# Performance work log

Hardware: AMD Instinct MI355X
Metric: run time of the kernel (lower is better)

## Reference

```python
import jax, jax.numpy as jnp
import numpy as np

BN = 100000
E = 1600000
C1 = 64
C2 = 64


def setup_inputs() -> dict:
    key = jax.random.key(0)
    k1, k2, k3, k4 = jax.random.split(key, 4)
    x = jax.random.normal(k1, (BN, C1), dtype=jnp.float32)
    e_ = jax.random.randint(k2, (2, E), 0, BN, dtype=jnp.int64)
    # nn.Linear(C1, C2): y = x @ W^T + b; store W pre-transposed as (C1, C2)
    W = jax.random.normal(k3, (C1, C2), dtype=jnp.float32) * (1.0 / np.sqrt(C1))
    b = jax.random.normal(k4, (C2,), dtype=jnp.float32) * 0.01
    return {"x": x, "e_": e_, "W": W, "b": b}


def reference(x, e_, W, b):
    bn = x.shape[0]
    row, col = e_[0], e_[1]
    # deg = bincount(row); deg^{-1/2} with inf -> 0
    deg = jax.ops.segment_sum(jnp.ones(row.shape, dtype=x.dtype), row, num_segments=bn)
    deg_inv_sqrt = jnp.where(deg > 0, jnp.power(jnp.maximum(deg, 1.0), -0.5), 0.0)
    norm = deg_inv_sqrt[row] * deg_inv_sqrt[col]          # (E,)
    h = x @ W + b                                         # (BN, C2)
    messages = norm[:, None] * h[row]                     # (E, C2) gather + scale
    y = jax.ops.segment_sum(messages, col, num_segments=bn)  # scatter-add over dst
    return y
```

## Files before the change

### kernel.cpp

```cpp
#include <hip/hip_runtime.h>
#include <hip/hip_bf16.h>

#define C 64
#define CPB 1024
#define NBUCK 98
#define EPB 4096
#define PAD 16
#define CAP 20480
#define NW 4

typedef __attribute__((ext_vector_type(8))) short bf16x8;
typedef __attribute__((ext_vector_type(4))) float f32x4;

__device__ __forceinline__ unsigned short f2bf(float f) {
    __hip_bfloat16 h = __float2bfloat16(f);
    return *(unsigned short*)&h;
}

__global__ void init_kernel(int* __restrict__ bcC, int* __restrict__ bcR) {
    int t = threadIdx.x;
    if (t < NBUCK) { bcC[t * PAD] = t * CAP; bcR[t * PAD] = t * CAP; }
}

__global__ __launch_bounds__(256) void partA_kernel(const int* __restrict__ row,
                                                    const int* __restrict__ col,
                                                    int* __restrict__ bcurC,
                                                    int* __restrict__ bcurR,
                                                    int* __restrict__ stageC,
                                                    unsigned short* __restrict__ stageR,
                                                    int ne) {
    __shared__ int cC[NW][NBUCK], cR[NW][NBUCK];
    const int tid = threadIdx.x;
    const int w = tid >> 6;
    for (int i = tid; i < NW * NBUCK; i += 256) { (&cC[0][0])[i] = 0; (&cR[0][0])[i] = 0; }
    __syncthreads();
    int s = blockIdx.x * EPB, e = min(s + EPB, ne);
    for (int i = s + tid; i < e; i += 256) {
        atomicAdd(&cC[w][col[i] >> 10], 1);
        atomicAdd(&cR[w][row[i] >> 10], 1);
    }
    __syncthreads();
    if (tid < NBUCK) {
        int tot = 0;
#pragma unroll
        for (int k = 0; k < NW; ++k) tot += cC[k][tid];
        int g = atomicAdd(&bcurC[tid * PAD], tot);
#pragma unroll
        for (int k = 0; k < NW; ++k) { int t2 = cC[k][tid]; cC[k][tid] = g; g += t2; }
        tot = 0;
#pragma unroll
        for (int k = 0; k < NW; ++k) tot += cR[k][tid];
        g = atomicAdd(&bcurR[tid * PAD], tot);
#pragma unroll
        for (int k = 0; k < NW; ++k) { int t2 = cR[k][tid]; cR[k][tid] = g; g += t2; }
    }
    __syncthreads();
    for (int i = s + tid; i < e; i += 256) {
        int r = row[i], c = col[i];
        int bk = c >> 10;
        int pos = atomicAdd(&cC[w][bk], 1);
        if (pos < (bk + 1) * CAP) stageC[pos] = ((c & (CPB - 1)) << 17) | r;
        int rb = r >> 10;
        int posR = atomicAdd(&cR[w][rb], 1);
        if (posR < (rb + 1) * CAP) stageR[posR] = (unsigned short)(r & (CPB - 1));
    }
}

__global__ void scanb_kernel(const int* __restrict__ bcC, int* __restrict__ bboff) {
    if (threadIdx.x == 0) {
        int acc = 0;
        for (int b = 0; b < NBUCK; ++b) {
            bboff[b] = acc;
            acc += bcC[b * PAD] - b * CAP;
        }
        bboff[NBUCK] = acc;
    }
}

__global__ __launch_bounds__(1024) void degB_kernel(const int* __restrict__ bcR,
                                                    const unsigned short* __restrict__ stageR,
                                                    float* __restrict__ dis, int bn) {
    __shared__ int hist[CPB];
    const int b = blockIdx.x, tid = threadIdx.x;
    hist[tid] = 0;
    __syncthreads();
    const int sb = b * CAP;
    const int cnt = bcR[b * PAD] - sb;
    for (int j = tid; j < cnt; j += 1024) atomicAdd(&hist[stageR[sb + j]], 1);
    __syncthreads();
    int r = b * CPB + tid;
    if (r < bn) {
        int d = hist[tid];
        dis[r] = d > 0 ? rsqrtf((float)d) : 0.0f;
    }
}

__global__ __launch_bounds__(1024) void partB_kernel(const int* __restrict__ bboff,
                                                     const int* __restrict__ stageC,
                                                     int* __restrict__ offs,
                                                     int* __restrict__ srcs,
                                                     int bn, int ne) {
    __shared__ int hist[CPB];
    __shared__ int wsum[16];
    const int b = blockIdx.x, tid = threadIdx.x;
    const int lane = tid & 63, wid = tid >> 6;
    hist[tid] = 0;
    __syncthreads();
    const int s = bboff[b];
    const int cnt = bboff[b + 1] - s;
    const int sb = b * CAP;
    for (int j = tid; j < cnt; j += 1024) atomicAdd(&hist[stageC[sb + j] >> 17], 1);
    __syncthreads();
    int v = hist[tid];
    int x = v;
#pragma unroll
    for (int off = 1; off < 64; off <<= 1) {
        int t = __shfl_up(x, off, 64);
        if (lane >= off) x += t;
    }
    if (lane == 63) wsum[wid] = x;
    __syncthreads();
    if (wid == 0) {
        int ws2 = (lane < 16) ? wsum[lane] : 0;
        int y = ws2;
#pragma unroll
        for (int off = 1; off < 16; off <<= 1) {
            int t = __shfl_up(y, off, 64);
            if (lane >= off) y += t;
        }
        if (lane < 16) wsum[lane] = y - ws2;
    }
    __syncthreads();
    int excl = (x - v) + wsum[wid];
    int c = b * CPB + tid;
    if (c < bn) offs[c] = s + excl;
    __syncthreads();
    hist[tid] = s + excl;
    __syncthreads();
    for (int j = tid; j < cnt; j += 1024) {
        int val = stageC[sb + j];
        int pos = atomicAdd(&hist[val >> 17], 1);
        srcs[pos] = val & 0x1FFFF;
    }
    if (b == NBUCK - 1 && tid == 0) offs[bn] = ne;
}

__global__ __launch_bounds__(256) void linear_mfma_kernel(const float* __restrict__ x,
                                                          const float* __restrict__ W,
                                                          const float* __restrict__ b,
                                                          const float* __restrict__ dis,
                                                          __hip_bfloat16* __restrict__ hb,
                                                          int bn) {
    __shared__ unsigned short xb[64][72];
    __shared__ unsigned short Wt[64][72];
    __shared__ float bs[64];
    __shared__ float dss[64];
    const int t = threadIdx.x;
    const int R0 = blockIdx.x * 64;

    {
        int row = t >> 2, q = t & 3;
        int grow = R0 + row;
        float4 vv[4];
        if (grow < bn) {
            const float4* xp = (const float4*)(x + (size_t)grow * C + q * 16);
#pragma unroll
            for (int i = 0; i < 4; ++i) vv[i] = xp[i];
        } else {
#pragma unroll
            for (int i = 0; i < 4; ++i) vv[i] = make_float4(0.f, 0.f, 0.f, 0.f);
        }
#pragma unroll
        for (int i = 0; i < 4; ++i) {
            unsigned short* d = &xb[row][q * 16 + i * 4];
            d[0] = f2bf(vv[i].x); d[1] = f2bf(vv[i].y);
            d[2] = f2bf(vv[i].z); d[3] = f2bf(vv[i].w);
        }
    }
    {
        int k = t >> 2, q = t & 3;
        const float* wp = W + (size_t)k * C + q * 16;
#pragma unroll
        for (int j = 0; j < 16; ++j) Wt[q * 16 + j][k] = f2bf(wp[j]);
    }
    if (t < 64) bs[t] = b[t];
    else if (t < 128) { int i = t - 64; int g = R0 + i; dss[i] = (g < bn) ? dis[g] : 0.f; }
    __syncthreads();

    const int wv = t >> 6;
    const int l = t & 63;
    const int lm = l & 15;
    const int g = l >> 4;

    const bf16x8 a0 = *(const bf16x8*)&xb[wv * 16 + lm][g * 8];
    const bf16x8 a1 = *(const bf16x8*)&xb[wv * 16 + lm][32 + g * 8];

#pragma unroll
    for (int n = 0; n < 4; ++n) {
        const bf16x8 b0 = *(const bf16x8*)&Wt[n * 16 + lm][g * 8];
        const bf16x8 b1 = *(const bf16x8*)&Wt[n * 16 + lm][32 + g * 8];
        float bias = bs[n * 16 + lm];
        f32x4 acc = {bias, bias, bias, bias};
        acc = __builtin_amdgcn_mfma_f32_16x16x32_bf16(a0, b0, acc, 0, 0, 0);
        acc = __builtin_amdgcn_mfma_f32_16x16x32_bf16(a1, b1, acc, 0, 0, 0);
#pragma unroll
        for (int reg = 0; reg < 4; ++reg) {
            int lrow = wv * 16 + g * 4 + reg;
            int grow = R0 + lrow;
            if (grow < bn)
                hb[(size_t)grow * C + n * 16 + lm] = __float2bfloat16(dss[lrow] * acc[reg]);
        }
    }
}

__device__ __forceinline__ float bf_lo(unsigned int p) { return __uint_as_float(p << 16); }
__device__ __forceinline__ float bf_hi(unsigned int p) { return __uint_as_float(p & 0xFFFF0000u); }

__global__ void gather_kernel(const int* __restrict__ offs, const int* __restrict__ srcs,
                              const uint2* __restrict__ hb64,
                              const float* __restrict__ dis,
                              float* __restrict__ y, int bn) {
    int r = blockIdx.x * (blockDim.x >> 6) + (threadIdx.x >> 6);
    if (r >= bn) return;
    const int lane = threadIdx.x & 63;
    const int q = lane >> 4;
    const int cq = lane & 15;
    const int s0 = offs[r], e0 = offs[r + 1];
    float4 acc = {0.f, 0.f, 0.f, 0.f};
    for (int base = s0; base < e0; base += 64) {
        int j = base + lane;
        int srcv = (j < e0) ? srcs[j] : 0;
        int cnt = min(64, e0 - base);
        int t = 0;
        for (; t + 16 <= cnt; t += 16) {
            int a0 = __shfl(srcv, t + q, 64);
            int a1 = __shfl(srcv, t + 4 + q, 64);
            int a2 = __shfl(srcv, t + 8 + q, 64);
            int a3 = __shfl(srcv, t + 12 + q, 64);
            uint2 p0 = hb64[(size_t)a0 * 16 + cq];
            uint2 p1 = hb64[(size_t)a1 * 16 + cq];
            uint2 p2 = hb64[(size_t)a2 * 16 + cq];
            uint2 p3 = hb64[(size_t)a3 * 16 + cq];
            acc.x += bf_lo(p0.x); acc.y += bf_hi(p0.x); acc.z += bf_lo(p0.y); acc.w += bf_hi(p0.y);
            acc.x += bf_lo(p1.x); acc.y += bf_hi(p1.x); acc.z += bf_lo(p1.y); acc.w += bf_hi(p1.y);
            acc.x += bf_lo(p2.x); acc.y += bf_hi(p2.x); acc.z += bf_lo(p2.y); acc.w += bf_hi(p2.y);
            acc.x += bf_lo(p3.x); acc.y += bf_hi(p3.x); acc.z += bf_lo(p3.y); acc.w += bf_hi(p3.y);
        }
        for (; t + 4 <= cnt; t += 4) {
            int a = __shfl(srcv, t + q, 64);
            uint2 p = hb64[(size_t)a * 16 + cq];
            acc.x += bf_lo(p.x); acc.y += bf_hi(p.x); acc.z += bf_lo(p.y); acc.w += bf_hi(p.y);
        }
        if (t < cnt) {
            int idx = t + q;
            int a = __shfl(srcv, idx & 63, 64);
            if (idx < cnt) {
                uint2 p = hb64[(size_t)a * 16 + cq];
                acc.x += bf_lo(p.x); acc.y += bf_hi(p.x); acc.z += bf_lo(p.y); acc.w += bf_hi(p.y);
            }
        }
    }
    acc.x += __shfl_xor(acc.x, 16, 64); acc.y += __shfl_xor(acc.y, 16, 64);
    acc.z += __shfl_xor(acc.z, 16, 64); acc.w += __shfl_xor(acc.w, 16, 64);
    acc.x += __shfl_xor(acc.x, 32, 64); acc.y += __shfl_xor(acc.y, 32, 64);
    acc.z += __shfl_xor(acc.z, 32, 64); acc.w += __shfl_xor(acc.w, 32, 64);
    if (q == 0) {
        float d = dis[r];
        float4 out = {acc.x * d, acc.y * d, acc.z * d, acc.w * d};
        *reinterpret_cast<float4*>(y + (size_t)r * C + 4 * cq) = out;
    }
}

extern "C" void kernel_launch(void* const* d_in, const int* in_sizes, int n_in,
                              void* d_out, int out_size, void* d_ws, size_t ws_size,
                              hipStream_t stream) {
    const float* x = (const float*)d_in[0];
    const int*   e = (const int*)d_in[1];
    const float* W = (const float*)d_in[2];
    const float* b = (const float*)d_in[3];
    float* y = (float*)d_out;

    const int bn = in_sizes[0] / C;
    const int ne = in_sizes[1] / 2;

    const int* rowi = e;
    const int* coli = e + ne;

    char* ws = (char*)d_ws;
    float* dis   = (float*)ws;  ws += (size_t)bn * 4;
    int*   offs  = (int*)ws;    ws += ((size_t)bn + 4) * 4;
    int*   bboff = (int*)ws;    ws += 512;
    int*   bcC   = (int*)ws;    ws += (size_t)NBUCK * PAD * 4;
    int*   bcR   = (int*)ws;    ws += (size_t)NBUCK * PAD * 4;
    int*   srcs  = (int*)ws;    ws += (size_t)ne * 4;
    __hip_bfloat16* hb = (__hip_bfloat16*)ws;
    int*            stageC = (int*)hb;
    unsigned short* stageR = (unsigned short*)((char*)hb + (size_t)NBUCK * CAP * 4);

    const int nchunks = (ne + EPB - 1) / EPB;
    init_kernel<<<1, 128, 0, stream>>>(bcC, bcR);
    partA_kernel<<<nchunks, 256, 0, stream>>>(rowi, coli, bcC, bcR, stageC, stageR, ne);
    degB_kernel<<<NBUCK, 1024, 0, stream>>>(bcR, stageR, dis, bn);
    scanb_kernel<<<1, 64, 0, stream>>>(bcC, bboff);
    partB_kernel<<<NBUCK, 1024, 0, stream>>>(bboff, stageC, offs, srcs, bn, ne);
    linear_mfma_kernel<<<(bn + 63) / 64, 256, 0, stream>>>(x, W, b, dis, hb, bn);
    gather_kernel<<<(bn + 3) / 4, 256, 0, stream>>>(offs, srcs, (const uint2*)hb, dis, y, bn);
}
```

Baseline: 148.5 us.

## Use finer 256-node buckets across partition, degree and CSR build kernels

Shrinks the bucket width from 1024 to 256 nodes, so there are 391 buckets instead of 98 and the degree and partB kernels launch four times as many smaller blocks. This is meant to fill more compute units during the bucket passes. PartA now preloads 16 edges per thread into registers, drops the per-wave counter copies, and stores row-degree staging as bytes. The serial single-thread bucket scan becomes a parallel wave scan. In exchange, more blocks contend on the same global bucket counters, and shared-memory atomics become more contended without the per-wave copies.

After: 135.1 us. -9.0%, faster.

```diff
diff --git a/kernel.cpp b/kernel.cpp
--- a/kernel.cpp
+++ b/kernel.cpp
@@ -2,12 +2,11 @@
 #include <hip/hip_bf16.h>
 
 #define C 64
-#define CPB 1024
-#define NBUCK 98
+#define CPB 256
+#define NBUCK 391
 #define EPB 4096
 #define PAD 16
-#define CAP 20480
-#define NW 4
+#define CAP 5120
 
 typedef __attribute__((ext_vector_type(8))) short bf16x8;
 typedef __attribute__((ext_vector_type(4))) float f32x4;
@@ -17,7 +16,7 @@
     return *(unsigned short*)&h;
 }
 
-__global__ void init_kernel(int* __restrict__ bcC, int* __restrict__ bcR) {
+__global__ __launch_bounds__(512) void init_kernel(int* __restrict__ bcC, int* __restrict__ bcR) {
     int t = threadIdx.x;
     if (t < NBUCK) { bcC[t * PAD] = t * CAP; bcR[t * PAD] = t * CAP; }
 }
@@ -27,66 +26,85 @@
                                                     int* __restrict__ bcurC,
                                                     int* __restrict__ bcurR,
                                                     int* __restrict__ stageC,
-                                                    unsigned short* __restrict__ stageR,
+                                                    unsigned char* __restrict__ stageR,
                                                     int ne) {
-    __shared__ int cC[NW][NBUCK], cR[NW][NBUCK];
+    __shared__ int cC[NBUCK], cR[NBUCK];
     const int tid = threadIdx.x;
-    const int w = tid >> 6;
-    for (int i = tid; i < NW * NBUCK; i += 256) { (&cC[0][0])[i] = 0; (&cR[0][0])[i] = 0; }
-    __syncthreads();
-    int s = blockIdx.x * EPB, e = min(s + EPB, ne);
-    for (int i = s + tid; i < e; i += 256) {
-        atomicAdd(&cC[w][col[i] >> 10], 1);
-        atomicAdd(&cR[w][row[i] >> 10], 1);
-    }
-    __syncthreads();
-    if (tid < NBUCK) {
-        int tot = 0;
-#pragma unroll
-        for (int k = 0; k < NW; ++k) tot += cC[k][tid];
-        int g = atomicAdd(&bcurC[tid * PAD], tot);
-#pragma unroll
-        for (int k = 0; k < NW; ++k) { int t2 = cC[k][tid]; cC[k][tid] = g; g += t2; }
-        tot = 0;
-#pragma unroll
-        for (int k = 0; k < NW; ++k) tot += cR[k][tid];
-        g = atomicAdd(&bcurR[tid * PAD], tot);
-#pragma unroll
-        for (int k = 0; k < NW; ++k) { int t2 = cR[k][tid]; cR[k][tid] = g; g += t2; }
-    }
-    __syncthreads();
-    for (int i = s + tid; i < e; i += 256) {
-        int r = row[i], c = col[i];
-        int bk = c >> 10;
-        int pos = atomicAdd(&cC[w][bk], 1);
-        if (pos < (bk + 1) * CAP) stageC[pos] = ((c & (CPB - 1)) << 17) | r;
-        int rb = r >> 10;
-        int posR = atomicAdd(&cR[w][rb], 1);
-        if (posR < (rb + 1) * CAP) stageR[posR] = (unsigned short)(r & (CPB - 1));
-    }
-}
-
-__global__ void scanb_kernel(const int* __restrict__ bcC, int* __restrict__ bboff) {
-    if (threadIdx.x == 0) {
-        int acc = 0;
-        for (int b = 0; b < NBUCK; ++b) {
-            bboff[b] = acc;
-            acc += bcC[b * PAD] - b * CAP;
-        }
-        bboff[NBUCK] = acc;
-    }
-}
-
-__global__ __launch_bounds__(1024) void degB_kernel(const int* __restrict__ bcR,
-                                                    const unsigned short* __restrict__ stageR,
-                                                    float* __restrict__ dis, int bn) {
+    for (int i = tid; i < NBUCK; i += 256) { cC[i] = 0; cR[i] = 0; }
+    __syncthreads();
+    const int s = blockIdx.x * EPB, e = min(s + EPB, ne);
+    int rr[16], cc[16];
+#pragma unroll
+    for (int u = 0; u < 16; ++u) {
+        int i = s + tid + u * 256;
+        if (i < e) { rr[u] = row[i]; cc[u] = col[i]; }
+        else { rr[u] = -1; cc[u] = -1; }
+    }
+#pragma unroll
+    for (int u = 0; u < 16; ++u) {
+        if (cc[u] >= 0) {
+            atomicAdd(&cC[cc[u] >> 8], 1);
+            atomicAdd(&cR[rr[u] >> 8], 1);
+        }
+    }
+    __syncthreads();
+    for (int t = tid; t < NBUCK; t += 256) {
+        int g = atomicAdd(&bcurC[t * PAD], cC[t]); cC[t] = g;
+        g = atomicAdd(&bcurR[t * PAD], cR[t]); cR[t] = g;
+    }
+    __syncthreads();
+#pragma unroll
+    for (int u = 0; u < 16; ++u) {
+        if (cc[u] >= 0) {
+            int bk = cc[u] >> 8;
+            int pos = atomicAdd(&cC[bk], 1);
+            if (pos < (bk + 1) * CAP) stageC[pos] = ((cc[u] & 255) << 17) | rr[u];
+            int rb = rr[u] >> 8;
+            int posR = atomicAdd(&cR[rb], 1);
+            if (posR < (rb + 1) * CAP) stageR[posR] = (unsigned char)(rr[u] & 255);
+        }
+    }
+}
+
+__global__ __launch_bounds__(512) void scanb_kernel(const int* __restrict__ bcC,
+                                                    int* __restrict__ bboff) {
+    __shared__ int wsum[8];
+    const int tid = threadIdx.x, lane = tid & 63, wid = tid >> 6;
+    int v = (tid < NBUCK) ? min(bcC[tid * PAD] - tid * CAP, CAP) : 0;
+    int x = v;
+#pragma unroll
+    for (int off = 1; off < 64; off <<= 1) {
+        int t = __shfl_up(x, off, 64);
+        if (lane >= off) x += t;
+    }
+    if (lane == 63) wsum[wid] = x;
+    __syncthreads();
+    if (wid == 0) {
+        int ws2 = (lane < 8) ? wsum[lane] : 0;
+        int y = ws2;
+#pragma unroll
+        for (int off = 1; off < 8; off <<= 1) {
+            int t = __shfl_up(y, off, 64);
+            if (lane >= off) y += t;
+        }
+        if (lane < 8) wsum[lane] = y - ws2;
+    }
+    __syncthreads();
+    int excl = (x - v) + wsum[wid];
+    if (tid < NBUCK) bboff[tid] = excl;
+    if (tid == NBUCK - 1) bboff[NBUCK] = excl + v;
+}
+
+__global__ __launch_bounds__(256) void degB_kernel(const int* __restrict__ bcR,
+                                                   const unsigned char* __restrict__ stageR,
+                                                   float* __restrict__ dis, int bn) {
     __shared__ int hist[CPB];
     const int b = blockIdx.x, tid = threadIdx.x;
     hist[tid] = 0;
     __syncthreads();
     const int sb = b * CAP;
-    const int cnt = bcR[b * PAD] - sb;
-    for (int j = tid; j < cnt; j += 1024) atomicAdd(&hist[stageR[sb + j]], 1);
+    const int cnt = min(bcR[b * PAD] - sb, CAP);
+    for (int j = tid; j < cnt; j += 256) atomicAdd(&hist[stageR[sb + j]], 1);
     __syncthreads();
     int r = b * CPB + tid;
     if (r < bn) {
@@ -95,23 +113,23 @@
     }
 }
 
-__global__ __launch_bounds__(1024) void partB_kernel(const int* __restrict__ bboff,
-                                                     const int* __restrict__ stageC,
-                                                     int* __restrict__ offs,
-                                                     int* __restrict__ srcs,
-                                                     int bn, int ne) {
+__global__ __launch_bounds__(512) void partB_kernel(const int* __restrict__ bboff,
+                                                    const int* __restrict__ stageC,
+                                                    int* __restrict__ offs,
+                                                    int* __restrict__ srcs,
+                                                    int bn, int ne) {
     __shared__ int hist[CPB];
-    __shared__ int wsum[16];
+    __shared__ int wsum[8];
     const int b = blockIdx.x, tid = threadIdx.x;
     const int lane = tid & 63, wid = tid >> 6;
-    hist[tid] = 0;
+    if (tid < CPB) hist[tid] = 0;
     __syncthreads();
     const int s = bboff[b];
     const int cnt = bboff[b + 1] - s;
     const int sb = b * CAP;
-    for (int j = tid; j < cnt; j += 1024) atomicAdd(&hist[stageC[sb + j] >> 17], 1);
-    __syncthreads();
-    int v = hist[tid];
+    for (int j = tid; j < cnt; j += 512) atomicAdd(&hist[stageC[sb + j] >> 17], 1);
+    __syncthreads();
+    int v = (tid < CPB) ? hist[tid] : 0;
     int x = v;
 #pragma unroll
     for (int off = 1; off < 64; off <<= 1) {
@@ -121,23 +139,23 @@
     if (lane == 63) wsum[wid] = x;
     __syncthreads();
     if (wid == 0) {
-        int ws2 = (lane < 16) ? wsum[lane] : 0;
+        int ws2 = (lane < 8) ? wsum[lane] : 0;
         int y = ws2;
 #pragma unroll
-        for (int off = 1; off < 16; off <<= 1) {
+        for (int off = 1; off < 8; off <<= 1) {
             int t = __shfl_up(y, off, 64);
             if (lane >= off) y += t;
         }
-        if (lane < 16) wsum[lane] = y - ws2;
+        if (lane < 8) wsum[lane] = y - ws2;
     }
     __syncthreads();
     int excl = (x - v) + wsum[wid];
     int c = b * CPB + tid;
-    if (c < bn) offs[c] = s + excl;
-    __syncthreads();
-    hist[tid] = s + excl;
-    __syncthreads();
-    for (int j = tid; j < cnt; j += 1024) {
+    if (tid < CPB && c < bn) offs[c] = s + excl;
+    __syncthreads();
+    if (tid < CPB) hist[tid] = s + excl;
+    __syncthreads();
+    for (int j = tid; j < cnt; j += 512) {
         int val = stageC[sb + j];
         int pos = atomicAdd(&hist[val >> 17], 1);
         srcs[pos] = val & 0x1FFFF;
@@ -289,20 +307,20 @@
     char* ws = (char*)d_ws;
     float* dis   = (float*)ws;  ws += (size_t)bn * 4;
     int*   offs  = (int*)ws;    ws += ((size_t)bn + 4) * 4;
-    int*   bboff = (int*)ws;    ws += 512;
+    int*   bboff = (int*)ws;    ws += ((size_t)NBUCK + 4) * 4;
     int*   bcC   = (int*)ws;    ws += (size_t)NBUCK * PAD * 4;
     int*   bcR   = (int*)ws;    ws += (size_t)NBUCK * PAD * 4;
     int*   srcs  = (int*)ws;    ws += (size_t)ne * 4;
     __hip_bfloat16* hb = (__hip_bfloat16*)ws;
-    int*            stageC = (int*)hb;
-    unsigned short* stageR = (unsigned short*)((char*)hb + (size_t)NBUCK * CAP * 4);
+    int*           stageC = (int*)hb;
+    unsigned char* stageR = (unsigned char*)((char*)hb + (size_t)NBUCK * CAP * 4);
 
     const int nchunks = (ne + EPB - 1) / EPB;
-    init_kernel<<<1, 128, 0, stream>>>(bcC, bcR);
+    init_kernel<<<1, 512, 0, stream>>>(bcC, bcR);
     partA_kernel<<<nchunks, 256, 0, stream>>>(rowi, coli, bcC, bcR, stageC, stageR, ne);
-    degB_kernel<<<NBUCK, 1024, 0, stream>>>(bcR, stageR, dis, bn);
-    scanb_kernel<<<1, 64, 0, stream>>>(bcC, bboff);
-    partB_kernel<<<NBUCK, 1024, 0, stream>>>(bboff, stageC, offs, srcs, bn, ne);
+    degB_kernel<<<NBUCK, 256, 0, stream>>>(bcR, stageR, dis, bn);
+    scanb_kernel<<<1, 512, 0, stream>>>(bcC, bboff);
+    partB_kernel<<<NBUCK, 512, 0, stream>>>(bboff, stageC, offs, srcs, bn, ne);
     linear_mfma_kernel<<<(bn + 63) / 64, 256, 0, stream>>>(x, W, b, dis, hb, bn);
     gather_kernel<<<(bn + 3) / 4, 256, 0, stream>>>(offs, srcs, (const uint2*)hb, dis, y, bn);
 }
```

## Use finer buckets and fuse degree, scan and CSR build into one kernel

Applied to the files above, without the earlier changes.

Shrinks the bucket size from 1024 to 128 nodes, giving 782 buckets and 8-bit local row indices in the degree stage. The degree computation, bucket-offset scan and CSR placement are merged into one kernel in which each block computes its own base offset by reducing the counts of earlier buckets. The init and scan kernels are replaced by a memset, partA uses a fixed 512-block grid of 512 threads, and the staging buffers get their own workspace region instead of aliasing hb. The aim is fewer launches and more parallel blocks in the CSR build, at the cost of more global atomics on bucket counters and a redundant prefix sum over earlier buckets in every block.

Result: no change. 150.9 us (+1.6%).

```diff
diff --git a/kernel.cpp b/kernel.cpp
--- a/kernel.cpp
+++ b/kernel.cpp
@@ -2,12 +2,10 @@
 #include <hip/hip_bf16.h>
 
 #define C 64
-#define CPB 1024
-#define NBUCK 98
-#define EPB 4096
+#define CPB 128
+#define NBUCK 782
 #define PAD 16
-#define CAP 20480
-#define NW 4
+#define CAP 2560
 
 typedef __attribute__((ext_vector_type(8))) short bf16x8;
 typedef __attribute__((ext_vector_type(4))) float f32x4;
@@ -17,132 +15,113 @@
     return *(unsigned short*)&h;
 }
 
-__global__ void init_kernel(int* __restrict__ bcC, int* __restrict__ bcR) {
-    int t = threadIdx.x;
-    if (t < NBUCK) { bcC[t * PAD] = t * CAP; bcR[t * PAD] = t * CAP; }
-}
-
-__global__ __launch_bounds__(256) void partA_kernel(const int* __restrict__ row,
+__global__ __launch_bounds__(512) void partA_kernel(const int* __restrict__ row,
                                                     const int* __restrict__ col,
                                                     int* __restrict__ bcurC,
                                                     int* __restrict__ bcurR,
                                                     int* __restrict__ stageC,
-                                                    unsigned short* __restrict__ stageR,
+                                                    unsigned char* __restrict__ stageR,
                                                     int ne) {
-    __shared__ int cC[NW][NBUCK], cR[NW][NBUCK];
+    __shared__ int cC[NBUCK], cR[NBUCK];
     const int tid = threadIdx.x;
-    const int w = tid >> 6;
-    for (int i = tid; i < NW * NBUCK; i += 256) { (&cC[0][0])[i] = 0; (&cR[0][0])[i] = 0; }
-    __syncthreads();
-    int s = blockIdx.x * EPB, e = min(s + EPB, ne);
-    for (int i = s + tid; i < e; i += 256) {
-        atomicAdd(&cC[w][col[i] >> 10], 1);
-        atomicAdd(&cR[w][row[i] >> 10], 1);
-    }
-    __syncthreads();
-    if (tid < NBUCK) {
-        int tot = 0;
-#pragma unroll
-        for (int k = 0; k < NW; ++k) tot += cC[k][tid];
-        int g = atomicAdd(&bcurC[tid * PAD], tot);
-#pragma unroll
-        for (int k = 0; k < NW; ++k) { int t2 = cC[k][tid]; cC[k][tid] = g; g += t2; }
-        tot = 0;
-#pragma unroll
-        for (int k = 0; k < NW; ++k) tot += cR[k][tid];
-        g = atomicAdd(&bcurR[tid * PAD], tot);
-#pragma unroll
-        for (int k = 0; k < NW; ++k) { int t2 = cR[k][tid]; cR[k][tid] = g; g += t2; }
-    }
-    __syncthreads();
-    for (int i = s + tid; i < e; i += 256) {
+    for (int i = tid; i < NBUCK; i += 512) { cC[i] = 0; cR[i] = 0; }
+    __syncthreads();
+    const int per = (ne + gridDim.x - 1) / gridDim.x;
+    const int s = blockIdx.x * per, e = min(s + per, ne);
+    for (int i = s + tid; i < e; i += 512) {
+        atomicAdd(&cC[col[i] >> 7], 1);
+        atomicAdd(&cR[row[i] >> 7], 1);
+    }
+    __syncthreads();
+    for (int t = tid; t < NBUCK; t += 512) {
+        int g = atomicAdd(&bcurC[t * PAD], cC[t]); cC[t] = t * CAP + g;
+        g = atomicAdd(&bcurR[t * PAD], cR[t]);     cR[t] = t * CAP + g;
+    }
+    __syncthreads();
+    for (int i = s + tid; i < e; i += 512) {
         int r = row[i], c = col[i];
-        int bk = c >> 10;
-        int pos = atomicAdd(&cC[w][bk], 1);
-        if (pos < (bk + 1) * CAP) stageC[pos] = ((c & (CPB - 1)) << 17) | r;
-        int rb = r >> 10;
-        int posR = atomicAdd(&cR[w][rb], 1);
-        if (posR < (rb + 1) * CAP) stageR[posR] = (unsigned short)(r & (CPB - 1));
-    }
-}
-
-__global__ void scanb_kernel(const int* __restrict__ bcC, int* __restrict__ bboff) {
-    if (threadIdx.x == 0) {
-        int acc = 0;
-        for (int b = 0; b < NBUCK; ++b) {
-            bboff[b] = acc;
-            acc += bcC[b * PAD] - b * CAP;
-        }
-        bboff[NBUCK] = acc;
-    }
-}
-
-__global__ __launch_bounds__(1024) void degB_kernel(const int* __restrict__ bcR,
-                                                    const unsigned short* __restrict__ stageR,
-                                                    float* __restrict__ dis, int bn) {
-    __shared__ int hist[CPB];
-    const int b = blockIdx.x, tid = threadIdx.x;
-    hist[tid] = 0;
-    __syncthreads();
-    const int sb = b * CAP;
-    const int cnt = bcR[b * PAD] - sb;
-    for (int j = tid; j < cnt; j += 1024) atomicAdd(&hist[stageR[sb + j]], 1);
-    __syncthreads();
-    int r = b * CPB + tid;
-    if (r < bn) {
-        int d = hist[tid];
-        dis[r] = d > 0 ? rsqrtf((float)d) : 0.0f;
-    }
-}
-
-__global__ __launch_bounds__(1024) void partB_kernel(const int* __restrict__ bboff,
+        int bk = c >> 7;
+        int pos = atomicAdd(&cC[bk], 1);
+        if (pos < (bk + 1) * CAP) stageC[pos] = ((c & 127) << 17) | r;
+        int rb = r >> 7;
+        int posR = atomicAdd(&cR[rb], 1);
+        if (posR < (rb + 1) * CAP) stageR[posR] = (unsigned char)(r & 127);
+    }
+}
+
+__global__ __launch_bounds__(512) void fusedB_kernel(const int* __restrict__ bcC,
+                                                     const int* __restrict__ bcR,
                                                      const int* __restrict__ stageC,
+                                                     const unsigned char* __restrict__ stageR,
+                                                     float* __restrict__ dis,
                                                      int* __restrict__ offs,
                                                      int* __restrict__ srcs,
                                                      int bn, int ne) {
     __shared__ int hist[CPB];
-    __shared__ int wsum[16];
+    __shared__ int wsum[8];
+    __shared__ int sbase_s;
     const int b = blockIdx.x, tid = threadIdx.x;
     const int lane = tid & 63, wid = tid >> 6;
-    hist[tid] = 0;
-    __syncthreads();
-    const int s = bboff[b];
-    const int cnt = bboff[b + 1] - s;
-    const int sb = b * CAP;
-    for (int j = tid; j < cnt; j += 1024) atomicAdd(&hist[stageC[sb + j] >> 17], 1);
-    __syncthreads();
-    int v = hist[tid];
-    int x = v;
-#pragma unroll
-    for (int off = 1; off < 64; off <<= 1) {
-        int t = __shfl_up(x, off, 64);
-        if (lane >= off) x += t;
-    }
-    if (lane == 63) wsum[wid] = x;
-    __syncthreads();
-    if (wid == 0) {
-        int ws2 = (lane < 16) ? wsum[lane] : 0;
-        int y = ws2;
-#pragma unroll
-        for (int off = 1; off < 16; off <<= 1) {
-            int t = __shfl_up(y, off, 64);
-            if (lane >= off) y += t;
-        }
-        if (lane < 16) wsum[lane] = y - ws2;
-    }
-    __syncthreads();
-    int excl = (x - v) + wsum[wid];
-    int c = b * CPB + tid;
-    if (c < bn) offs[c] = s + excl;
-    __syncthreads();
-    hist[tid] = s + excl;
-    __syncthreads();
-    for (int j = tid; j < cnt; j += 1024) {
-        int val = stageC[sb + j];
+
+    if (tid < CPB) hist[tid] = 0;
+    __syncthreads();
+    const int sbR = b * CAP;
+    const int cntR = min(bcR[b * PAD], CAP);
+    for (int j = tid; j < cntR; j += 512) atomicAdd(&hist[stageR[sbR + j]], 1);
+    __syncthreads();
+    {
+        int r = b * CPB + tid;
+        if (tid < CPB && r < bn) {
+            int d = hist[tid];
+            dis[r] = d > 0 ? rsqrtf((float)d) : 0.0f;
+        }
+    }
+    int part = 0;
+    for (int t = tid; t < b; t += 512) part += min(bcC[t * PAD], CAP);
+#pragma unroll
+    for (int off = 32; off >= 1; off >>= 1) part += __shfl_xor(part, off, 64);
+    if (lane == 0) wsum[wid] = part;
+    __syncthreads();
+    if (tid == 0) {
+        int s = 0;
+#pragma unroll
+        for (int k = 0; k < 8; ++k) s += wsum[k];
+        sbase_s = s;
+    }
+    __syncthreads();
+    const int sbase = sbase_s;
+    __syncthreads();
+    if (tid < CPB) hist[tid] = 0;
+    __syncthreads();
+    const int sbC = b * CAP;
+    const int cntC = min(bcC[b * PAD], CAP);
+    for (int j = tid; j < cntC; j += 512) atomicAdd(&hist[stageC[sbC + j] >> 17], 1);
+    __syncthreads();
+    int v = 0, x = 0;
+    if (tid < CPB) {
+        v = hist[tid];
+        x = v;
+#pragma unroll
+        for (int off = 1; off < 64; off <<= 1) {
+            int t = __shfl_up(x, off, 64);
+            if (lane >= off) x += t;
+        }
+        if (lane == 63) wsum[wid] = x;
+    }
+    __syncthreads();
+    if (tid < CPB) {
+        int excl = (x - v) + (wid == 1 ? wsum[0] : 0);
+        int c = b * CPB + tid;
+        if (c < bn) offs[c] = sbase + excl;
+        hist[tid] = sbase + excl;
+    }
+    __syncthreads();
+    for (int j = tid; j < cntC; j += 512) {
+        int val = stageC[sbC + j];
         int pos = atomicAdd(&hist[val >> 17], 1);
         srcs[pos] = val & 0x1FFFF;
     }
-    if (b == NBUCK - 1 && tid == 0) offs[bn] = ne;
+    if (b == NBUCK - 1 && tid == 0) offs[bn] = sbase + cntC;
 }
 
 __global__ __launch_bounds__(256) void linear_mfma_kernel(const float* __restrict__ x,
@@ -289,20 +268,17 @@
     char* ws = (char*)d_ws;
     float* dis   = (float*)ws;  ws += (size_t)bn * 4;
     int*   offs  = (int*)ws;    ws += ((size_t)bn + 4) * 4;
-    int*   bboff = (int*)ws;    ws += 512;
     int*   bcC   = (int*)ws;    ws += (size_t)NBUCK * PAD * 4;
     int*   bcR   = (int*)ws;    ws += (size_t)NBUCK * PAD * 4;
     int*   srcs  = (int*)ws;    ws += (size_t)ne * 4;
+    int*           stageC = (int*)ws;           ws += (size_t)NBUCK * CAP * 4;
+    unsigned char* stageR = (unsigned char*)ws; ws += (size_t)NBUCK * CAP;
     __hip_bfloat16* hb = (__hip_bfloat16*)ws;
-    int*            stageC = (int*)hb;
-    unsigned short* stageR = (unsigned short*)((char*)hb + (size_t)NBUCK * CAP * 4);
-
-    const int nchunks = (ne + EPB - 1) / EPB;
-    init_kernel<<<1, 128, 0, stream>>>(bcC, bcR);
-    partA_kernel<<<nchunks, 256, 0, stream>>>(rowi, coli, bcC, bcR, stageC, stageR, ne);
-    degB_kernel<<<NBUCK, 1024, 0, stream>>>(bcR, stageR, dis, bn);
-    scanb_kernel<<<1, 64, 0, stream>>>(bcC, bboff);
-    partB_kernel<<<NBUCK, 1024, 0, stream>>>(bboff, stageC, offs, srcs, bn, ne);
+
+    hipMemsetAsync(bcC, 0, (size_t)NBUCK * PAD * 8, stream);
+
+    partA_kernel<<<512, 512, 0, stream>>>(rowi, coli, bcC, bcR, stageC, stageR, ne);
+    fusedB_kernel<<<NBUCK, 512, 0, stream>>>(bcC, bcR, stageC, stageR, dis, offs, srcs, bn, ne);
     linear_mfma_kernel<<<(bn + 63) / 64, 256, 0, stream>>>(x, W, b, dis, hb, bn);
     gather_kernel<<<(bn + 3) / 4, 256, 0, stream>>>(offs, srcs, (const uint2*)hb, dis, y, bn);
 }
```
